# Optimization experiments

Measured on AMD Instinct MI355X. Metric: run time of the kernel, lower is better.

## Reference

```python
import jax, jax.numpy as jnp
import numpy as np

B, S, C, H, E, K = 8, 512, 768, 12, 8, 2
MLP_H = int(C * 4.0)
HD = C // H
ROUTER_REG = 0.01
LN_EPS = 1e-5


def setup_inputs() -> dict:
    key = jax.random.key(0)
    ks = jax.random.split(key, 8)

    def w(k, shape, fan_in):
        return (jax.random.normal(k, shape, dtype=jnp.float32) / np.sqrt(fan_in)).astype(jnp.float32)

    return {
        "x": jax.random.normal(ks[0], (B, S, C), dtype=jnp.float32),
        "expert_tokens": w(ks[1], (E, C), C),
        "ln1_g": jnp.ones((E, C), jnp.float32),
        "ln1_b": jnp.zeros((E, C), jnp.float32),
        "qkv_w": w(ks[2], (E, C, 3 * C), C),
        "qkv_b": jnp.zeros((E, 3 * C), jnp.float32),
        "proj_w": w(ks[3], (E, C, C), C),
        "proj_b": jnp.zeros((E, C), jnp.float32),
        "ln2_g": jnp.ones((E, C), jnp.float32),
        "ln2_b": jnp.zeros((E, C), jnp.float32),
        "fc1_w": w(ks[4], (E, C, MLP_H), C),
        "fc1_b": jnp.zeros((E, MLP_H), jnp.float32),
        "fc2_w": w(ks[5], (E, MLP_H, C), MLP_H),
        "fc2_b": jnp.zeros((E, C), jnp.float32),
    }


def _layernorm(x, g, b):
    mu = jnp.mean(x, axis=-1, keepdims=True)
    var = jnp.mean(jnp.square(x - mu), axis=-1, keepdims=True)
    return (x - mu) * jax.lax.rsqrt(var + LN_EPS) * g + b


def _block(x, p):
    # One transformer Block (pre-LN attention + MLP), params for a single expert.
    ln1_g, ln1_b, qkv_w, qkv_b, proj_w, proj_b, ln2_g, ln2_b, fc1_w, fc1_b, fc2_w, fc2_b = p
    h = _layernorm(x, ln1_g, ln1_b)
    qkv = (h @ qkv_w + qkv_b).reshape(B, S, 3, H, HD)
    q, k, v = qkv[:, :, 0], qkv[:, :, 1], qkv[:, :, 2]  # [B,S,H,HD]
    # NOTE: original code MULTIPLIES by sqrt(head_dim) (scale = head_dim**0.5).
    scale = jnp.float32(np.sqrt(HD))
    attn = jax.nn.softmax(jnp.einsum('bqhd,bkhd->bhqk', q, k) * scale, axis=-1)
    o = jnp.einsum('bhqk,bkhd->bqhd', attn, v).reshape(B, S, C)
    x = x + (o @ proj_w + proj_b)
    h2 = _layernorm(x, ln2_g, ln2_b)
    x = x + (jax.nn.gelu(h2 @ fc1_w + fc1_b, approximate=False) @ fc2_w + fc2_b)
    return x


def reference(x, expert_tokens, ln1_g, ln1_b, qkv_w, qkv_b, proj_w, proj_b,
              ln2_g, ln2_b, fc1_w, fc1_b, fc2_w, fc2_b):
    # Router
    router_logits = jnp.einsum('bsc,nc->bsn', x, expert_tokens) / jnp.float32(np.sqrt(C))
    router_probs = jax.nn.softmax(router_logits, axis=-1)
    top_k_probs, top_k_idx = jax.lax.top_k(router_probs, K)  # [B,S,K]
    top_k_probs = top_k_probs / jnp.sum(top_k_probs, axis=-1, keepdims=True)

    # Dense all-expert compute (sequential over experts to bound memory)
    params = (ln1_g, ln1_b, qkv_w, qkv_b, proj_w, proj_b, ln2_g, ln2_b,
              fc1_w, fc1_b, fc2_w, fc2_b)
    expert_out = jax.lax.map(lambda p: _block(x, p), params)  # [E,B,S,C]
    expert_out = jnp.transpose(expert_out, (1, 2, 0, 3))       # [B,S,E,C]

    # Top-k gather and weighted combine
    sel = jnp.take_along_axis(expert_out, top_k_idx[..., None], axis=2)  # [B,S,K,C]
    combine = jnp.sum(sel * top_k_probs[..., None], axis=2)
    out = x + combine

    # Load-balance auxiliary loss
    counts = jnp.sum(jax.nn.one_hot(top_k_idx, E, dtype=jnp.float32), axis=(0, 1, 2))
    f_i = counts / jnp.float32(B * S * K)
    P_i = jnp.mean(router_probs, axis=(0, 1))
    balance_loss = E * jnp.sum(f_i * P_i) + ROUTER_REG * jnp.linalg.norm(expert_tokens)
    return out, balance_loss
```

## Files before the change

### kernel.cpp

```cpp
#include <hip/hip_runtime.h>
#include <hip/hip_bf16.h>

#define BB 8
#define SS 512
#define CC 768
#define HH 12
#define HD 64
#define EE 8
#define KK 2
#define MLPH 3072
#define NT (BB*SS)
#define NOUT (NT*CC)

#define SLOTB      68059136ull
#define SLOT_U16   34029568ull
#define SLOT_F32   17014784ull

typedef unsigned int u32;
typedef unsigned short u16;
typedef __attribute__((ext_vector_type(8))) short short8;
typedef __attribute__((ext_vector_type(4))) float f32x4;

__device__ __forceinline__ u16 f2bf(float f) {
    u32 u = __builtin_bit_cast(u32, f);
    u32 r = (u + 0x7fffu + ((u >> 16) & 1u)) >> 16;
    return (u16)r;
}
__device__ __forceinline__ float bf2f(u16 h) {
    u32 u = ((u32)h) << 16;
    return __builtin_bit_cast(float, u);
}
__device__ __forceinline__ void gl_lds16(const void* g, void* l) {
    __builtin_amdgcn_global_load_lds(
        (const __attribute__((address_space(1))) u32*)g,
        (__attribute__((address_space(3))) u32*)l, 16, 0, 0);
}
__device__ __forceinline__ void swz_rc(int bid, int& bm, int& bn) {
    int xcd = bid & 7, off = bid >> 3;
    bm = (xcd * 4 + (off & 3)) * 128;
    bn = (off >> 2) * 128;
}

__device__ __forceinline__ void stage128x64(const u16* __restrict__ G, size_t ldg,
                                            u16* s, int tid)
{
    int wid = tid >> 6, lane = tid & 63;
#pragma unroll
    for (int it = 0; it < 4; ++it) {
        int cb = it * 256 + wid * 64;
        int c = cb + lane;
        int row = c >> 3;
        int ch = (c & 7) ^ (row & 7);
        gl_lds16(G + (size_t)row * ldg + ch * 8, s + cb * 8);
    }
}
__device__ __forceinline__ short8 frag64(const u16* s, int row, int kc, int lb) {
    int ch = (kc * 4 + lb) ^ (row & 7);
    return *(const short8*)(s + row * 64 + ch * 8);
}

__global__ __launch_bounds__(256) void router_kernel(const float* __restrict__ x,
    const float* __restrict__ et, float* __restrict__ W, float* __restrict__ stats)
{
    __shared__ float etl[EE * CC];
    __shared__ float pred[4][2 * EE];
    int tid = threadIdx.x;
    for (int i = tid; i < EE * CC; i += 256) etl[i] = et[i];
    __syncthreads();
    int wid = tid >> 6, lane = tid & 63;
    float psum[EE] = {}, csum[EE] = {};
    for (int i = 0; i < 2; i++) {
        int t = blockIdx.x * 8 + wid * 2 + i;
        const float* xr = x + (size_t)t * CC;
        float acc[EE] = {};
        for (int c = lane; c < CC; c += 64) {
            float xv = xr[c];
#pragma unroll
            for (int e = 0; e < EE; e++) acc[e] += xv * etl[e * CC + c];
        }
#pragma unroll
        for (int e = 0; e < EE; e++)
            for (int off = 1; off < 64; off <<= 1) acc[e] += __shfl_xor(acc[e], off, 64);
        if (lane == 0) {
            const float inv = 0.03608439182435161f;
            float l[EE], m = -1e30f;
#pragma unroll
            for (int e = 0; e < EE; e++) { l[e] = acc[e] * inv; m = fmaxf(m, l[e]); }
            float p[EE], sum = 0.f;
#pragma unroll
            for (int e = 0; e < EE; e++) { p[e] = __expf(l[e] - m); sum += p[e]; }
            int i1 = 0;
#pragma unroll
            for (int e = 1; e < EE; e++) if (p[e] > p[i1]) i1 = e;
            int i2 = -1;
#pragma unroll
            for (int e = 0; e < EE; e++) if (e != i1 && (i2 < 0 || p[e] > p[i2])) i2 = e;
            float wn = p[i1] + p[i2];
#pragma unroll
            for (int e = 0; e < EE; e++) W[t * EE + e] = 0.f;
            W[t * EE + i1] = p[i1] / wn;
            W[t * EE + i2] = p[i2] / wn;
#pragma unroll
            for (int e = 0; e < EE; e++) psum[e] += p[e] / sum;
            csum[i1] += 1.f; csum[i2] += 1.f;
        }
    }
    if (lane == 0) {
#pragma unroll
        for (int e = 0; e < EE; e++) { pred[wid][e] = psum[e]; pred[wid][EE + e] = csum[e]; }
    }
    __syncthreads();
    if (tid < 2 * EE) {
        float s = pred[0][tid] + pred[1][tid] + pred[2][tid] + pred[3][tid];
        atomicAdd(&stats[tid], s);
    }
}

template<int MODE>
__global__ __launch_bounds__(256) void ln_kernel(const float* __restrict__ x, size_t xslot,
    u16* __restrict__ out_hi, u16* __restrict__ out_lo, size_t oslot)
{
    int t = blockIdx.x;
    int eb = blockIdx.y;
    const float* xr = x + (size_t)eb * xslot + (size_t)t * CC;
    __shared__ float red[256];
    int tid = threadIdx.x;
    float v[3];
    float s = 0.f;
#pragma unroll
    for (int i = 0; i < 3; i++) { v[i] = xr[tid + i * 256]; s += v[i]; }
    red[tid] = s; __syncthreads();
    for (int off = 128; off > 0; off >>= 1) { if (tid < off) red[tid] += red[tid + off]; __syncthreads(); }
    float mu = red[0] / (float)CC;
    __syncthreads();
    float s2 = 0.f;
#pragma unroll
    for (int i = 0; i < 3; i++) { float d = v[i] - mu; s2 += d * d; }
    red[tid] = s2; __syncthreads();
    for (int off = 128; off > 0; off >>= 1) { if (tid < off) red[tid] += red[tid + off]; __syncthreads(); }
    float var = red[0] / (float)CC;
    float sc = rsqrtf(var + 1e-5f);
#pragma unroll
    for (int i = 0; i < 3; i++) {
        int c = tid + i * 256;
        float val = (v[i] - mu) * sc;
        u16 hi = f2bf(val);
        out_hi[(size_t)eb * oslot + (size_t)t * CC + c] = hi;
        if (MODE) out_lo[(size_t)eb * oslot + (size_t)t * CC + c] = f2bf(val - bf2f(hi));
    }
}

__global__ __launch_bounds__(256) void prep_expert(
    const float* __restrict__ qkv_w0, const float* __restrict__ qkv_b0,
    const float* __restrict__ proj_w0,
    const float* __restrict__ fc1_w0, const float* __restrict__ fc1_b0,
    const float* __restrict__ fc2_w0,
    const float* __restrict__ g1_0, const float* __restrict__ b1_0,
    const float* __restrict__ g2_0, const float* __restrict__ b2_0,
    u16* __restrict__ qkvTh, u16* __restrict__ qkvTl,
    u16* __restrict__ projT, u16* __restrict__ fc1T, u16* __restrict__ fc2T,
    float* __restrict__ biasq, float* __restrict__ biasf1, int ebase)
{
    __shared__ float tile[32][33];
    __shared__ float bsh[CC];
    __shared__ float redg[256];
    int bid = blockIdx.x;
    int eb = blockIdx.y;
    int ge = ebase + eb;
    int tid = threadIdx.x;
    const float* qkv_w = qkv_w0 + (size_t)ge * CC * 3 * CC;
    const float* qkv_b = qkv_b0 + (size_t)ge * 3 * CC;
    const float* proj_w = proj_w0 + (size_t)ge * CC * CC;
    const float* fc1_w = fc1_w0 + (size_t)ge * CC * MLPH;
    const float* fc1_b = fc1_b0 + (size_t)ge * MLPH;
    const float* fc2_w = fc2_w0 + (size_t)ge * MLPH * CC;
    const float* g1 = g1_0 + (size_t)ge * CC;
    const float* b1 = b1_0 + (size_t)ge * CC;
    const float* g2 = g2_0 + (size_t)ge * CC;
    const float* b2 = b2_0 + (size_t)ge * CC;

    if (bid < 6912) {
        const float* src; const float* scale = nullptr;
        u16 *dh, *dl = nullptr; int N, Kd, n0, k0;
        if (bid < 1728) {
            src = qkv_w; scale = g1;
            dh = qkvTh + (size_t)eb * SLOT_U16; dl = qkvTl + (size_t)eb * SLOT_U16;
            N = 2304; Kd = 768; n0 = (bid % 72) * 32; k0 = (bid / 72) * 32;
        } else if (bid < 2304) {
            int i = bid - 1728;
            src = proj_w; dh = projT + (size_t)eb * SLOT_U16; N = 768; Kd = 768;
            n0 = (i % 24) * 32; k0 = (i / 24) * 32;
        } else if (bid < 4608) {
            int i = bid - 2304;
            src = fc1_w; scale = g2; dh = fc1T + (size_t)eb * SLOT_U16; N = 3072; Kd = 768;
            n0 = (i % 96) * 32; k0 = (i / 96) * 32;
        } else {
            int i = bid - 4608;
            src = fc2_w; dh = fc2T + (size_t)eb * SLOT_U16; N = 768; Kd = 3072;
            n0 = (i % 24) * 32; k0 = (i / 24) * 32;
        }
        int tx = tid & 31, ty = tid >> 5;
#pragma unroll
        for (int i = 0; i < 32; i += 8) {
            float v = src[(size_t)(k0 + ty + i) * N + n0 + tx];
            if (scale) v *= scale[k0 + ty + i];
            tile[ty + i][tx] = v;
        }
        __syncthreads();
#pragma unroll
        for (int i = 0; i < 32; i += 8) {
            float v = tile[tx][ty + i];
            u16 hi = f2bf(v);
            dh[(size_t)(n0 + ty + i) * Kd + k0 + tx] = hi;
            if (dl) dl[(size_t)(n0 + ty + i) * Kd + k0 + tx] = f2bf(v - bf2f(hi));
        }
    } else {
        const float* bv; const float* wsrc; const float* badd;
        float* dst; int N, n0;
        if (bid < 6984) { bv = b1; wsrc = qkv_w; badd = qkv_b; dst = biasq + (size_t)eb * SLOT_F32; N = 2304; n0 = (bid - 6912) * 32; }
        else            { bv = b2; wsrc = fc1_w; badd = fc1_b; dst = biasf1 + (size_t)eb * SLOT_F32; N = MLPH; n0 = (bid - 6984) * 32; }
        for (int i = tid; i < CC; i += 256) bsh[i] = bv[i];
        __syncthreads();
        int g = tid & 31, l8 = tid >> 5;
        int n = n0 + g;
        float acc = 0.f;
        for (int k = l8; k < CC; k += 8) acc += bsh[k] * wsrc[(size_t)k * N + n];
        redg[tid] = acc; __syncthreads();
        if (tid < 32) {
            float sum = 0.f;
#pragma unroll
            for (int i = 0; i < 8; i++) sum += redg[tid + i * 32];
            dst[n0 + tid] = sum + badd[n0 + tid];
        }
    }
}

__global__ __launch_bounds__(256) void gemm_qkv_bk64(
    const u16* __restrict__ Ah, const u16* __restrict__ Al,
    const u16* __restrict__ Bh0, const u16* __restrict__ Bl0,
    const float* __restrict__ biasq0, u16* __restrict__ qk_hi0,
    u16* __restrict__ qk_lo0, u16* __restrict__ vtout0)
{
    __shared__ __align__(16) u16 sAh[128 * 64], sAl[128 * 64];
    __shared__ __align__(16) u16 sBh[128 * 64], sBl[128 * 64];
    int tid = threadIdx.x;
    int eb = blockIdx.y;
    int bm, bn;
    swz_rc(blockIdx.x, bm, bn);
    bool qk_tile = (bn < 1536);
    int wid = tid >> 6, lane = tid & 63;
    int wr = wid >> 1, wc = wid & 1;
    int la = lane & 15, lb = lane >> 4;
    const u16* Bh = Bh0 + (size_t)eb * SLOT_U16;
    const u16* Bl = Bl0 + (size_t)eb * SLOT_U16;
    const float* bias = biasq0 + (size_t)eb * SLOT_F32;
    u16* qk_hi = qk_hi0 + (size_t)eb * SLOT_U16;
    u16* qk_lo = qk_lo0 + (size_t)eb * SLOT_U16;
    u16* vtout = vtout0 + (size_t)eb * SLOT_U16;

    f32x4 acc[4][4];
#pragma unroll
    for (int i = 0; i < 4; i++)
#pragma unroll
        for (int j = 0; j < 4; j++) acc[i][j] = (f32x4){0.f, 0.f, 0.f, 0.f};

    const u16* Abh = Ah + (size_t)bm * CC;
    const u16* Abl = Al + (size_t)bm * CC;
    const u16* Bbh = Bh + (size_t)bn * CC;
    const u16* Bbl = Bl + (size_t)bn * CC;
    for (int k0 = 0; k0 < CC; k0 += 64) {
        stage128x64(Abh + k0, CC, sAh, tid);
        stage128x64(Bbh + k0, CC, sBh, tid);
        if (qk_tile) {
            stage128x64(Abl + k0, CC, sAl, tid);
            stage128x64(Bbl + k0, CC, sBl, tid);
        }
        __syncthreads();
        if (qk_tile) {
#pragma unroll
            for (int kc = 0; kc < 2; kc++) {
                short8 avh[4], avl[4], bvh[4], bvl[4];
#pragma unroll
                for (int i = 0; i < 4; i++) {
                    int row = wr * 64 + i * 16 + la;
                    avh[i] = frag64(sAh, row, kc, lb);
                    avl[i] = frag64(sAl, row, kc, lb);
                }
#pragma unroll
                for (int j = 0; j < 4; j++) {
                    int row = wc * 64 + j * 16 + la;
                    bvh[j] = frag64(sBh, row, kc, lb);
                    bvl[j] = frag64(sBl, row, kc, lb);
                }
#pragma unroll
                for (int i = 0; i < 4; i++)
#pragma unroll
                    for (int j = 0; j < 4; j++) {
                        acc[i][j] = __builtin_amdgcn_mfma_f32_16x16x32_bf16(avh[i], bvh[j], acc[i][j], 0, 0, 0);
                        acc[i][j] = __builtin_amdgcn_mfma_f32_16x16x32_bf16(avh[i], bvl[j], acc[i][j], 0, 0, 0);
                        acc[i][j] = __builtin_amdgcn_mfma_f32_16x16x32_bf16(avl[i], bvh[j], acc[i][j], 0, 0, 0);
                    }
            }
        } else {
#pragma unroll
            for (int kc = 0; kc < 2; kc++) {
                short8 avh[4], bvh[4];
#pragma unroll
                for (int i = 0; i < 4; i++) avh[i] = frag64(sAh, wr * 64 + i * 16 + la, kc, lb);
#pragma unroll
                for (int j = 0; j < 4; j++) bvh[j] = frag64(sBh, wc * 64 + j * 16 + la, kc, lb);
#pragma unroll
                for (int i = 0; i < 4; i++)
#pragma unroll
                    for (int j = 0; j < 4; j++)
                        acc[i][j] = __builtin_amdgcn_mfma_f32_16x16x32_bf16(avh[i], bvh[j], acc[i][j], 0, 0, 0);
            }
        }
        __syncthreads();
    }
#pragma unroll
    for (int i = 0; i < 4; i++) {
#pragma unroll
        for (int j = 0; j < 4; j++) {
            int gn = bn + wc * 64 + j * 16 + la;
            float bsv = bias[gn];
#pragma unroll
            for (int r = 0; r < 4; r++) {
                int gm = bm + wr * 64 + i * 16 + lb * 4 + r;
                float v = acc[i][j][r] + bsv;
                if (gn < 1536) {
                    u16 hi = f2bf(v);
                    qk_hi[(size_t)gm * 1536 + gn] = hi;
                    qk_lo[(size_t)gm * 1536 + gn] = f2bf(v - bf2f(hi));
                } else {
                    int dd = (gn - 1536) & 63, hh = (gn - 1536) >> 6;
                    int ss = gm & (SS - 1), bb = gm >> 9;
                    vtout[((size_t)((bb * HH + hh) * HD + dd)) * SS + ss] = f2bf(v);
                }
            }
        }
    }
}

template<int EPI>
__global__ __launch_bounds__(256) void gemm_b(
    const u16* __restrict__ A, size_t Aslot,
    const u16* __restrict__ BT, size_t Bslot,
    const float* __restrict__ bias, size_t biasSlot,
    const float* __restrict__ res, size_t resSlot,
    const float* __restrict__ Wt, int ebase,
    const float* __restrict__ xinit,
    void* __restrict__ Cout, size_t CoutSlot, int N, int Kdim)
{
    __shared__ __align__(16) u16 sA[2][128 * 64];
    __shared__ __align__(16) u16 sB[2][128 * 64];
    int tid = threadIdx.x;
    int eb = blockIdx.y;
    int ge = ebase + eb;
    int bm, bn;
    swz_rc(blockIdx.x, bm, bn);
    int wid = tid >> 6, lane = tid & 63;
    int wr = wid >> 1, wc = wid & 1;
    int la = lane & 15, lb = lane >> 4;
    f32x4 acc[4][4];
#pragma unroll
    for (int i = 0; i < 4; i++)
#pragma unroll
        for (int j = 0; j < 4; j++) acc[i][j] = (f32x4){0.f, 0.f, 0.f, 0.f};

    const u16* Ab = A + (size_t)eb * Aslot + (size_t)bm * Kdim;
    const u16* Bb = BT + (size_t)eb * Bslot + (size_t)bn * Kdim;
    stage128x64(Ab, Kdim, sA[0], tid);
    stage128x64(Bb, Kdim, sB[0], tid);
    __syncthreads();
    int cur = 0;
    for (int k0 = 0; k0 < Kdim; k0 += 64) {
        if (k0 + 64 < Kdim) {
            stage128x64(Ab + k0 + 64, Kdim, sA[cur ^ 1], tid);
            stage128x64(Bb + k0 + 64, Kdim, sB[cur ^ 1], tid);
        }
#pragma unroll
        for (int kc = 0; kc < 2; kc++) {
            short8 av[4], bv[4];
#pragma unroll
            for (int i = 0; i < 4; i++) av[i] = frag64(sA[cur], wr * 64 + i * 16 + la, kc, lb);
#pragma unroll
            for (int j = 0; j < 4; j++) bv[j] = frag64(sB[cur], wc * 64 + j * 16 + la, kc, lb);
#pragma unroll
            for (int i = 0; i < 4; i++)
#pragma unroll
                for (int j = 0; j < 4; j++)
                    acc[i][j] = __builtin_amdgcn_mfma_f32_16x16x32_bf16(av[i], bv[j], acc[i][j], 0, 0, 0);
        }
        __syncthreads();
        cur ^= 1;
    }
    const float* biasp = bias + (size_t)eb * biasSlot;
    const float* resp = res ? res + (size_t)eb * resSlot : nullptr;
#pragma unroll
    for (int i = 0; i < 4; i++) {
#pragma unroll
        for (int j = 0; j < 4; j++) {
            int gn = bn + wc * 64 + j * 16 + la;
            float bsv = biasp[gn];
#pragma unroll
            for (int r = 0; r < 4; r++) {
                int gm = bm + wr * 64 + i * 16 + lb * 4 + r;
                size_t idx = (size_t)gm * N + gn;
                float v = acc[i][j][r];
                if (EPI == 1) {
                    ((float*)Cout + (size_t)eb * CoutSlot)[idx] = resp[idx] + v + bsv;
                } else if (EPI == 2) {
                    v += bsv;
                    float gel = 0.5f * v * (1.0f + erff(v * 0.70710678118654752f));
                    ((u16*)Cout + (size_t)eb * CoutSlot)[idx] = f2bf(gel);
                } else {
                    float w = Wt[(size_t)gm * EE + ge];
                    float val = w * (v + bsv + resp[idx]);
                    if (ge == 0) val += xinit[idx];
                    atomicAdd(&((float*)Cout)[idx], val);
                }
            }
        }
    }
}

__global__ __launch_bounds__(256) void attn_mfma(const u16* __restrict__ qk_hi0,
    const u16* __restrict__ qk_lo0, const u16* __restrict__ vt0, u16* __restrict__ o0)
{
    int q0 = blockIdx.x * 64;
    int h = blockIdx.y;
    int z = blockIdx.z;
    int b = z & (BB - 1), eb = z >> 3;
    int tid = threadIdx.x, wid = tid >> 6, lane = tid & 63;
    int la = lane & 15, lb = lane >> 4;
    __shared__ __align__(16) u16 Ksh[2][64 * 64];
    __shared__ __align__(16) u16 Ksl[2][64 * 64];
    __shared__ __align__(16) u16 Vs[2][64 * 64];
    __shared__ __align__(16) u16 Ps[4][16 * 64];

    const u16* qk_hi = qk_hi0 + (size_t)eb * SLOT_U16;
    const u16* qk_lo = qk_lo0 + (size_t)eb * SLOT_U16;
    const u16* vt = vt0 + (size_t)eb * SLOT_U16;
    u16* o = o0 + (size_t)eb * SLOT_U16;

    short8 aqh[2], aql[2];
    {
        size_t qoff = (size_t)(b * SS + q0 + wid * 16 + la) * 1536 + h * HD;
#pragma unroll
        for (int kc = 0; kc < 2; kc++) {
            aqh[kc] = *(const short8*)(qk_hi + qoff + kc * 32 + lb * 8);
            aql[kc] = *(const short8*)(qk_lo + qoff + kc * 32 + lb * 8);
        }
    }
    const u16* kbh = qk_hi + (size_t)(b * SS) * 1536 + CC + h * HD;
    const u16* kbl = qk_lo + (size_t)(b * SS) * 1536 + CC + h * HD;
    const u16* vtbase = vt + (size_t)((b * HH + h) * HD) * SS;

    float m_r[4], l_r[4];
    f32x4 acc_o[4];
#pragma unroll
    for (int r = 0; r < 4; r++) { m_r[r] = -1e30f; l_r[r] = 0.f; }
#pragma unroll
    for (int d0 = 0; d0 < 4; d0++) acc_o[d0] = (f32x4){0.f, 0.f, 0.f, 0.f};

    auto STAGE = [&](int buf, int kt) {
#pragma unroll
        for (int it = 0; it < 2; it++) {
            int base = it * 256 + wid * 64;
            int c = base + lane;
            int row = c >> 3;
            int gk = (c & 7) ^ (row & 7);
            gl_lds16(kbh + (size_t)(kt + row) * 1536 + gk * 8, &Ksh[buf][base * 8]);
            gl_lds16(kbl + (size_t)(kt + row) * 1536 + gk * 8, &Ksl[buf][base * 8]);
            gl_lds16(vtbase + (size_t)row * SS + kt + gk * 8, &Vs[buf][base * 8]);
        }
    };

    STAGE(0, 0);
    __syncthreads();
    int cur = 0;
    for (int kt = 0; kt < SS; kt += 64) {
        if (kt + 64 < SS) STAGE(cur ^ 1, kt + 64);

        f32x4 s4[4];
#pragma unroll
        for (int j = 0; j < 4; j++) s4[j] = (f32x4){0.f, 0.f, 0.f, 0.f};
#pragma unroll
        for (int kc = 0; kc < 2; kc++)
#pragma unroll
            for (int j = 0; j < 4; j++) {
                size_t off = (size_t)(j * 16 + la) * 64 + (((kc * 4 + lb) ^ (la & 7)) * 8);
                short8 bkh = *(const short8*)(&Ksh[cur][off]);
                short8 bkl = *(const short8*)(&Ksl[cur][off]);
                s4[j] = __builtin_amdgcn_mfma_f32_16x16x32_bf16(aqh[kc], bkh, s4[j], 0, 0, 0);
                s4[j] = __builtin_amdgcn_mfma_f32_16x16x32_bf16(aql[kc], bkh, s4[j], 0, 0, 0);
                s4[j] = __builtin_amdgcn_mfma_f32_16x16x32_bf16(aqh[kc], bkl, s4[j], 0, 0, 0);
            }
#pragma unroll
        for (int j = 0; j < 4; j++) s4[j] = s4[j] * 8.f;

#pragma unroll
        for (int r = 0; r < 4; r++) {
            float mx = fmaxf(fmaxf(s4[0][r], s4[1][r]), fmaxf(s4[2][r], s4[3][r]));
#pragma unroll
            for (int off = 1; off < 16; off <<= 1) mx = fmaxf(mx, __shfl_xor(mx, off, 64));
            float mn = fmaxf(m_r[r], mx);
            float corr = __expf(m_r[r] - mn);
            m_r[r] = mn;
            float rs = 0.f;
#pragma unroll
            for (int j = 0; j < 4; j++) {
                float p = __expf(s4[j][r] - mn);
                s4[j][r] = p; rs += p;
            }
#pragma unroll
            for (int off = 1; off < 16; off <<= 1) rs += __shfl_xor(rs, off, 64);
            l_r[r] = l_r[r] * corr + rs;
#pragma unroll
            for (int d0 = 0; d0 < 4; d0++) acc_o[d0][r] = acc_o[d0][r] * corr;
        }
#pragma unroll
        for (int j = 0; j < 4; j++)
#pragma unroll
            for (int r = 0; r < 4; r++) {
                int row = lb * 4 + r;
                int sg = (2 * j + (la >> 3)) ^ (row & 7);
                Ps[wid][row * 64 + sg * 8 + (la & 7)] = f2bf(s4[j][r]);
            }
        short8 pa[2];
#pragma unroll
        for (int kc = 0; kc < 2; kc++)
            pa[kc] = *(const short8*)(&Ps[wid][la * 64 + (((kc * 4 + lb) ^ (la & 7)) * 8)]);
#pragma unroll
        for (int d0 = 0; d0 < 4; d0++)
#pragma unroll
            for (int kc = 0; kc < 2; kc++) {
                short8 bv = *(const short8*)(&Vs[cur][(d0 * 16 + la) * 64 + (((kc * 4 + lb) ^ (la & 7)) * 8)]);
                acc_o[d0] = __builtin_amdgcn_mfma_f32_16x16x32_bf16(pa[kc], bv, acc_o[d0], 0, 0, 0);
            }
        __syncthreads();
        cur ^= 1;
    }
#pragma unroll
    for (int r = 0; r < 4; r++) {
        float invl = 1.f / l_r[r];
        int tok = b * SS + q0 + wid * 16 + lb * 4 + r;
#pragma unroll
        for (int d0 = 0; d0 < 4; d0++)
            o[(size_t)tok * CC + h * HD + d0 * 16 + la] = f2bf(acc_o[d0][r] * invl);
    }
}

__global__ __launch_bounds__(256) void loss_kernel(const float* __restrict__ et,
    const float* __restrict__ stats, float* __restrict__ out_loss)
{
    __shared__ float red[256];
    int tid = threadIdx.x;
    float s = 0.f;
    for (int i = tid; i < EE * CC; i += 256) { float v = et[i]; s += v * v; }
    red[tid] = s; __syncthreads();
    for (int off = 128; off > 0; off >>= 1) { if (tid < off) red[tid] += red[tid + off]; __syncthreads(); }
    if (tid == 0) {
        float bl = 0.f;
        for (int e = 0; e < EE; e++) {
            float f = stats[EE + e] / (float)(NT * KK);
            float P = stats[e] / (float)NT;
            bl += f * P;
        }
        *out_loss = (float)EE * bl + 0.01f * sqrtf(red[0]);
    }
}

extern "C" void kernel_launch(void* const* d_in, const int* in_sizes, int n_in,
                              void* d_out, int out_size, void* d_ws, size_t ws_size,
                              hipStream_t stream) {
    const float* x      = (const float*)d_in[0];
    const float* et     = (const float*)d_in[1];
    const float* ln1_g  = (const float*)d_in[2];
    const float* ln1_b  = (const float*)d_in[3];
    const float* qkv_w  = (const float*)d_in[4];
    const float* qkv_b  = (const float*)d_in[5];
    const float* proj_w = (const float*)d_in[6];
    const float* proj_b = (const float*)d_in[7];
    const float* ln2_g  = (const float*)d_in[8];
    const float* ln2_b  = (const float*)d_in[9];
    const float* fc1_w  = (const float*)d_in[10];
    const float* fc1_b  = (const float*)d_in[11];
    const float* fc2_w  = (const float*)d_in[12];
    const float* fc2_b  = (const float*)d_in[13];
    float* outp = (float*)d_out;
    char* base = (char*)d_ws;

    const size_t FIXED = 12714496;
    int EB = 1;
    if (ws_size >= FIXED + 8 * SLOTB) EB = 8;
    else if (ws_size >= FIXED + 4 * SLOTB) EB = 4;
    else if (ws_size >= FIXED + 2 * SLOTB) EB = 2;

    float* W      = (float*)(base);
    float* stats  = (float*)(base + 131072);
    u16*   xh_hi  = (u16*)  (base + 131584);
    u16*   xh_lo  = (u16*)  (base + 6423040);
    char* slot0 = base + FIXED;
    u16*   qkvTh  = (u16*)  (slot0);
    u16*   qkvTl  = (u16*)  (slot0 + 3538944);
    u16*   projT  = (u16*)  (slot0 + 7077888);
    u16*   fc1T   = (u16*)  (slot0 + 8257536);
    u16*   fc2T   = (u16*)  (slot0 + 12976128);
    float* biasq  = (float*)(slot0 + 17694720);
    float* biasf1 = (float*)(slot0 + 17711104);
    u16*   qk_hi  = (u16*)  (slot0 + 17727488);
    u16*   qk_lo  = (u16*)  (slot0 + 30310400);
    u16*   mlp1   = (u16*)  (slot0 + 17727488);
    u16*   vtb    = (u16*)  (slot0 + 42893312);
    u16*   xmhat  = (u16*)  (slot0 + 42893312);
    u16*   obf    = (u16*)  (slot0 + 49184768);
    float* xmid   = (float*)(slot0 + 55476224);

    hipMemsetAsync(stats, 0, 16 * sizeof(float), stream);
    hipMemsetAsync(outp, 0, (size_t)NOUT * sizeof(float), stream);

    router_kernel<<<NT / 8, 256, 0, stream>>>(x, et, W, stats);
    ln_kernel<1><<<dim3(NT, 1), 256, 0, stream>>>(x, 0, xh_hi, xh_lo, 0);

    for (int ebase = 0; ebase < EE; ebase += EB) {
        prep_expert<<<dim3(7080, EB), 256, 0, stream>>>(
            qkv_w, qkv_b, proj_w, fc1_w, fc1_b, fc2_w,
            ln1_g, ln1_b, ln2_g, ln2_b,
            qkvTh, qkvTl, projT, fc1T, fc2T, biasq, biasf1, ebase);

        gemm_qkv_bk64<<<dim3(18 * 32, EB), 256, 0, stream>>>(
            xh_hi, xh_lo, qkvTh, qkvTl, biasq, qk_hi, qk_lo, vtb);

        attn_mfma<<<dim3(SS / 64, HH, BB * EB), 256, 0, stream>>>(qk_hi, qk_lo, vtb, obf);

        gemm_b<1><<<dim3(6 * 32, EB), 256, 0, stream>>>(
            obf, SLOT_U16, projT, SLOT_U16, proj_b + (size_t)ebase * CC, CC,
            x, 0, nullptr, 0, nullptr, xmid, SLOT_F32, CC, CC);

        ln_kernel<0><<<dim3(NT, EB), 256, 0, stream>>>(xmid, SLOT_F32, xmhat, nullptr, SLOT_U16);

        gemm_b<2><<<dim3(24 * 32, EB), 256, 0, stream>>>(
            xmhat, SLOT_U16, fc1T, SLOT_U16, biasf1, SLOT_F32,
            nullptr, 0, nullptr, 0, nullptr, mlp1, SLOT_U16, MLPH, CC);

        gemm_b<5><<<dim3(6 * 32, EB), 256, 0, stream>>>(
            mlp1, SLOT_U16, fc2T, SLOT_U16, fc2_b + (size_t)ebase * CC, CC,
            xmid, SLOT_F32, W, ebase, x, outp, 0, CC, MLPH);
    }

    loss_kernel<<<1, 256, 0, stream>>>(et, stats, outp + NOUT);
}
```

Before: 1.650 ms.

## Drop LDS double buffering in GEMM and attention kernels

Replaces the double-buffered shared-memory staging in the bf16 GEMM and flash-attention kernels with single buffers, loading each tile and then synchronising before compute. This halves LDS usage per block, which may allow more resident blocks per CU and so more occupancy-based latency hiding. In exchange, global-to-LDS loads no longer overlap with MFMA compute inside a block, and every tile pays a full load-then-wait stall.

```diff
diff --git a/kernel.cpp b/kernel.cpp
--- a/kernel.cpp
+++ b/kernel.cpp
@@ -352,8 +352,8 @@
     const float* __restrict__ xinit,
     void* __restrict__ Cout, size_t CoutSlot, int N, int Kdim)
 {
-    __shared__ __align__(16) u16 sA[2][128 * 64];
-    __shared__ __align__(16) u16 sB[2][128 * 64];
+    __shared__ __align__(16) u16 sA[128 * 64];
+    __shared__ __align__(16) u16 sB[128 * 64];
     int tid = threadIdx.x;
     int eb = blockIdx.y;
     int ge = ebase + eb;
@@ -370,22 +370,17 @@
 
     const u16* Ab = A + (size_t)eb * Aslot + (size_t)bm * Kdim;
     const u16* Bb = BT + (size_t)eb * Bslot + (size_t)bn * Kdim;
-    stage128x64(Ab, Kdim, sA[0], tid);
-    stage128x64(Bb, Kdim, sB[0], tid);
-    __syncthreads();
-    int cur = 0;
     for (int k0 = 0; k0 < Kdim; k0 += 64) {
-        if (k0 + 64 < Kdim) {
-            stage128x64(Ab + k0 + 64, Kdim, sA[cur ^ 1], tid);
-            stage128x64(Bb + k0 + 64, Kdim, sB[cur ^ 1], tid);
-        }
+        stage128x64(Ab + k0, Kdim, sA, tid);
+        stage128x64(Bb + k0, Kdim, sB, tid);
+        __syncthreads();
 #pragma unroll
         for (int kc = 0; kc < 2; kc++) {
             short8 av[4], bv[4];
 #pragma unroll
-            for (int i = 0; i < 4; i++) av[i] = frag64(sA[cur], wr * 64 + i * 16 + la, kc, lb);
-#pragma unroll
-            for (int j = 0; j < 4; j++) bv[j] = frag64(sB[cur], wc * 64 + j * 16 + la, kc, lb);
+            for (int i = 0; i < 4; i++) av[i] = frag64(sA, wr * 64 + i * 16 + la, kc, lb);
+#pragma unroll
+            for (int j = 0; j < 4; j++) bv[j] = frag64(sB, wc * 64 + j * 16 + la, kc, lb);
 #pragma unroll
             for (int i = 0; i < 4; i++)
 #pragma unroll
@@ -393,7 +388,6 @@
                     acc[i][j] = __builtin_amdgcn_mfma_f32_16x16x32_bf16(av[i], bv[j], acc[i][j], 0, 0, 0);
         }
         __syncthreads();
-        cur ^= 1;
     }
     const float* biasp = bias + (size_t)eb * biasSlot;
     const float* resp = res ? res + (size_t)eb * resSlot : nullptr;
@@ -434,9 +428,9 @@
     int b = z & (BB - 1), eb = z >> 3;
     int tid = threadIdx.x, wid = tid >> 6, lane = tid & 63;
     int la = lane & 15, lb = lane >> 4;
-    __shared__ __align__(16) u16 Ksh[2][64 * 64];
-    __shared__ __align__(16) u16 Ksl[2][64 * 64];
-    __shared__ __align__(16) u16 Vs[2][64 * 64];
+    __shared__ __align__(16) u16 Ksh[64 * 64];
+    __shared__ __align__(16) u16 Ksl[64 * 64];
+    __shared__ __align__(16) u16 Vs[64 * 64];
     __shared__ __align__(16) u16 Ps[4][16 * 64];
 
     const u16* qk_hi = qk_hi0 + (size_t)eb * SLOT_U16;
@@ -464,24 +458,18 @@
 #pragma unroll
     for (int d0 = 0; d0 < 4; d0++) acc_o[d0] = (f32x4){0.f, 0.f, 0.f, 0.f};
 
-    auto STAGE = [&](int buf, int kt) {
+    for (int kt = 0; kt < SS; kt += 64) {
 #pragma unroll
         for (int it = 0; it < 2; it++) {
             int base = it * 256 + wid * 64;
             int c = base + lane;
             int row = c >> 3;
             int gk = (c & 7) ^ (row & 7);
-            gl_lds16(kbh + (size_t)(kt + row) * 1536 + gk * 8, &Ksh[buf][base * 8]);
-            gl_lds16(kbl + (size_t)(kt + row) * 1536 + gk * 8, &Ksl[buf][base * 8]);
-            gl_lds16(vtbase + (size_t)row * SS + kt + gk * 8, &Vs[buf][base * 8]);
-        }
-    };
-
-    STAGE(0, 0);
-    __syncthreads();
-    int cur = 0;
-    for (int kt = 0; kt < SS; kt += 64) {
-        if (kt + 64 < SS) STAGE(cur ^ 1, kt + 64);
+            gl_lds16(kbh + (size_t)(kt + row) * 1536 + gk * 8, Ksh + base * 8);
+            gl_lds16(kbl + (size_t)(kt + row) * 1536 + gk * 8, Ksl + base * 8);
+            gl_lds16(vtbase + (size_t)row * SS + kt + gk * 8, Vs + base * 8);
+        }
+        __syncthreads();
 
         f32x4 s4[4];
 #pragma unroll
@@ -491,8 +479,8 @@
 #pragma unroll
             for (int j = 0; j < 4; j++) {
                 size_t off = (size_t)(j * 16 + la) * 64 + (((kc * 4 + lb) ^ (la & 7)) * 8);
-                short8 bkh = *(const short8*)(&Ksh[cur][off]);
-                short8 bkl = *(const short8*)(&Ksl[cur][off]);
+                short8 bkh = *(const short8*)(Ksh + off);
+                short8 bkl = *(const short8*)(Ksl + off);
                 s4[j] = __builtin_amdgcn_mfma_f32_16x16x32_bf16(aqh[kc], bkh, s4[j], 0, 0, 0);
                 s4[j] = __builtin_amdgcn_mfma_f32_16x16x32_bf16(aql[kc], bkh, s4[j], 0, 0, 0);
                 s4[j] = __builtin_amdgcn_mfma_f32_16x16x32_bf16(aqh[kc], bkl, s4[j], 0, 0, 0);
@@ -536,11 +524,10 @@
         for (int d0 = 0; d0 < 4; d0++)
 #pragma unroll
             for (int kc = 0; kc < 2; kc++) {
-                short8 bv = *(const short8*)(&Vs[cur][(d0 * 16 + la) * 64 + (((kc * 4 + lb) ^ (la & 7)) * 8)]);
+                short8 bv = *(const short8*)(&Vs[(d0 * 16 + la) * 64 + (((kc * 4 + lb) ^ (la & 7)) * 8)]);
                 acc_o[d0] = __builtin_amdgcn_mfma_f32_16x16x32_bf16(pa[kc], bv, acc_o[d0], 0, 0, 0);
             }
         __syncthreads();
-        cur ^= 1;
     }
 #pragma unroll
     for (int r = 0; r < 4; r++) {
```

New measurement: 1.566 ms. -5.1%, faster.
